# Optimization experiments

Hardware: AMD Instinct MI355X
Metric: run time of the kernel (lower is better)

## Reference

```python
import jax, jax.numpy as jnp
import numpy as np

B, QUE, VAL, D = 4, 128, 128, 512

def setup_inputs() -> dict:
    key = jax.random.key(0)
    k = jax.random.split(key, 8)
    return {
        "qs_1": jax.random.normal(k[0], (B, QUE, D), jnp.float32),
        "qs_2": jax.random.normal(k[1], (B, QUE, D), jnp.float32),  # unused by forward, kept for signature fidelity
        "ks":   jax.random.normal(k[2], (B, VAL, D), jnp.float32),
        "vs":   jax.random.normal(k[3], (B, VAL, D), jnp.float32),
        "sg_mask": jax.random.randint(k[4], (B, VAL), 0, 2).astype(bool),  # True = masked
        "W1":  jax.random.normal(k[5], (D, D), jnp.float32) / np.sqrt(D),
        "b1":  jnp.zeros((D,), jnp.float32),
        "Wse": jax.random.normal(k[6], (D, D), jnp.float32) / np.sqrt(D),
        "bse": jnp.zeros((D,), jnp.float32),
        "W2":  jax.random.normal(k[7], (D, 1), jnp.float32) / np.sqrt(D),
        "b2":  jnp.zeros((1,), jnp.float32),
    }

def reference(qs_1, qs_2, ks, vs, sg_mask, W1, b1, Wse, bse, W2, b2):
    # Pairwise query-key elementwise product: [B, que, val, d]
    x = qs_1[:, :, None, :] * ks[:, None, :, :]
    # linear1: Linear(d,d) + ReLU (dropout = identity at eval)
    h = jax.nn.relu(jnp.einsum('bqvd,de->bqve', x, W1) + b1)
    # linear2: Linear(d,1) + ReLU -> scalar score per (q, v) pair
    s = jax.nn.relu(jnp.einsum('bqvd,do->bqvo', h, W2) + b2)[..., 0]  # [B, que, val]
    m = sg_mask[:, None, :]                      # [B, 1, val], True = masked out
    # masked mean of h over the val axis (masked_fill(0) then divide by valid count)
    h = jnp.where(m[..., None], 0.0, h)
    denom = jnp.sum(~sg_mask, axis=-1).astype(h.dtype)      # [B]
    mean = h.sum(axis=2) / denom[:, None, None]             # [B, que, d]
    # squeeze-excitation gate: sigmoid(relu(Linear(d,d)))
    gate = jax.nn.sigmoid(jax.nn.relu(mean @ Wse + bse))    # [B, que, d]
    # masked softmax over val, weighted sum of values
    s = jnp.where(m, -1e9, s)
    w = jax.nn.softmax(s, axis=-1)                          # [B, que, val]
    out = jnp.einsum('bqv,bvd->bqd', w, vs)                 # [B, que, d]
    return gate * out
```

## Files before the change

kernel.cpp:

```cpp
#include <hip/hip_runtime.h>
#include <stdint.h>
#include <stddef.h>

#define BDIM 4
#define QUE  128
#define VAL  128
#define DD   512
#define BQ   (BDIM*QUE)
#define BK   64

typedef float    f32x4 __attribute__((ext_vector_type(4)));
typedef float    f32x2 __attribute__((ext_vector_type(2)));
typedef _Float16 f16x8 __attribute__((ext_vector_type(8)));
typedef _Float16 f16x4 __attribute__((ext_vector_type(4)));
typedef _Float16 f16x2 __attribute__((ext_vector_type(2)));

typedef const __attribute__((address_space(1))) void* gas_ptr;
typedef __attribute__((address_space(3))) void*       las_ptr;

__device__ __forceinline__ void async_copy16(const void* g, void* l) {
    __builtin_amdgcn_global_load_lds((gas_ptr)g, (las_ptr)l, 16, 0, 0);
}

__global__ __launch_bounds__(256) void prep_kernel(const float* __restrict__ W1,
                                                   _Float16* __restrict__ W1T,
                                                   const float* __restrict__ Wse,
                                                   _Float16* __restrict__ WseT,
                                                   const float* __restrict__ vs,
                                                   _Float16* __restrict__ vsT,
                                                   const float* __restrict__ qs1,
                                                   _Float16* __restrict__ qH,
                                                   const float* __restrict__ ks,
                                                   _Float16* __restrict__ ksH) {
    const int gx = blockIdx.x, gy = blockIdx.y;
    if (gy >= 36) {
        const float* src = (gy == 36) ? qs1 : ks;
        _Float16*    dst = (gy == 36) ? qH  : ksH;
        size_t base = (size_t)gx * 16384 + threadIdx.x * 4;
        #pragma unroll 4
        for (int i = 0; i < 16; ++i) {
            f32x4 w = *(const f32x4*)(src + base + (size_t)i * 1024);
            f16x4 h;
            h[0] = (_Float16)w[0]; h[1] = (_Float16)w[1];
            h[2] = (_Float16)w[2]; h[3] = (_Float16)w[3];
            *(f16x4*)(dst + base + (size_t)i * 1024) = h;
        }
        return;
    }
    __shared__ float tile[32][33];
    const int tx = threadIdx.x & 31;
    const int ty = threadIdx.x >> 5;
    if (gy < 32) {
        const float* src = (gy < 16) ? W1  : Wse;
        _Float16*    dst = (gy < 16) ? W1T : WseT;
        int a0 = gx * 32;
        int b0 = (gy & 15) * 32;
        #pragma unroll
        for (int r = 0; r < 4; ++r)
            tile[ty + r*8][tx] = src[(size_t)(a0 + ty + r*8) * DD + b0 + tx];
        __syncthreads();
        #pragma unroll
        for (int r = 0; r < 4; ++r) {
            int el = ty + r*8;
            dst[(size_t)(b0 + el) * DD + a0 + tx] = (_Float16)tile[tx][el];
        }
    } else {
        int bb = gy - 32;
        const float* src = vs  + (size_t)bb * VAL * DD;
        _Float16*    dst = vsT + (size_t)bb * DD * VAL;
        int b0 = gx * 32;
        for (int vt = 0; vt < 4; ++vt) {
            int a0 = vt * 32;
            __syncthreads();
            #pragma unroll
            for (int r = 0; r < 4; ++r)
                tile[ty + r*8][tx] = src[(size_t)(a0 + ty + r*8) * DD + b0 + tx];
            __syncthreads();
            #pragma unroll
            for (int r = 0; r < 4; ++r) {
                int el = ty + r*8;
                dst[(size_t)(b0 + el) * VAL + a0 + tx] = (_Float16)tile[tx][el];
            }
        }
    }
}

__global__ __launch_bounds__(256, 3) void gemm_h_kernel(
    const _Float16* __restrict__ qH,
    const _Float16* __restrict__ ksH,
    const int*   __restrict__ sgmask,
    const _Float16* __restrict__ W1T,
    const float* __restrict__ b1,
    const float* __restrict__ W2,
    float* __restrict__ s_part,
    float* __restrict__ meansum)
{
    __shared__ _Float16 Ah[2][128 * BK];
    __shared__ _Float16 Bh[128 * BK];
    __shared__ float sred[2][VAL];
    __shared__ float msumLDS[2][128];

    const int tid  = threadIdx.x;
    const int bq   = blockIdx.x;
    const int gy   = blockIdx.y;
    const int b    = bq >> 7;
    const int lane = tid & 63;
    const int wid  = tid >> 6;
    const int wm   = wid >> 1;
    const int wn   = wid & 1;
    const int quad = lane >> 4;
    const int lr   = lane & 15;

    f32x4 acc[4][4];
    #pragma unroll
    for (int i = 0; i < 4; ++i)
        #pragma unroll
        for (int j = 0; j < 4; ++j) acc[i][j] = (f32x4){0.f, 0.f, 0.f, 0.f};

    const int ar0 = tid >> 3;
    const int slt = tid & 7;
    const int ca0 = (slt - (ar0 & 7)) & 7;
    const _Float16* ksrow0 = ksH + ((size_t)b * VAL + ar0) * DD + ca0 * 8;
    const _Float16* qrow_g = qH  + (size_t)bq * DD + ca0 * 8;
    const int aoff0 = tid * 8;

    const int brow0 = tid >> 3;
    const int bc0   = ((tid & 7) - (brow0 & 7)) & 7;
    const _Float16* gB0 = W1T + (size_t)(gy * 128 + brow0) * DD + bc0 * 8;

    int faoff[4], fboff[4];
    #pragma unroll
    for (int mt = 0; mt < 4; ++mt) {
        int row = wm * 64 + mt * 16 + lr;
        faoff[mt] = row * BK + (((quad + row) & 7) << 3);
    }
    #pragma unroll
    for (int nt = 0; nt < 4; ++nt) {
        int row = wn * 64 + nt * 16 + lr;
        fboff[nt] = row * BK + (((quad + row) & 7) << 3);
    }

    #pragma unroll
    for (int j = 0; j < 4; ++j)
        async_copy16(gB0 + (size_t)j * 32 * DD, &Bh[(j * 256 + wid * 64) * 8]);
    f16x8 kv[4], qv;
    #pragma unroll
    for (int j = 0; j < 4; ++j)
        kv[j] = *(const f16x8*)(ksrow0 + (size_t)j * 32 * DD);
    qv = *(const f16x8*)(qrow_g);
    #pragma unroll
    for (int j = 0; j < 4; ++j)
        *(f16x8*)&Ah[0][aoff0 + j * 2048] = kv[j] * qv;
    #pragma unroll
    for (int j = 0; j < 4; ++j)
        kv[j] = *(const f16x8*)(ksrow0 + (size_t)j * 32 * DD + BK);
    qv = *(const f16x8*)(qrow_g + BK);
    __syncthreads();

    int p = 0;
    for (int i = 0; i < 8; ++i) {
        f16x8 fbr[2][4];
        #pragma unroll
        for (int s = 0; s < 2; ++s) {
            const int sx = s << 5;
            #pragma unroll
            for (int nt = 0; nt < 4; ++nt)
                fbr[s][nt] = *(const f16x8*)&Bh[fboff[nt] ^ sx];
        }
        asm volatile("s_waitcnt lgkmcnt(0)" ::: "memory");
        __builtin_amdgcn_s_barrier();

        if (i < 7) {
            const int kk = (i + 1) * BK;
            #pragma unroll
            for (int j = 0; j < 4; ++j)
                *(f16x8*)&Ah[p ^ 1][aoff0 + j * 2048] = kv[j] * qv;
            if (i < 6) {
                #pragma unroll
                for (int j = 0; j < 4; ++j)
                    kv[j] = *(const f16x8*)(ksrow0 + (size_t)j * 32 * DD + kk + BK);
                qv = *(const f16x8*)(qrow_g + kk + BK);
            }
            #pragma unroll
            for (int j = 0; j < 4; ++j)
                async_copy16(gB0 + (size_t)j * 32 * DD + kk,
                             &Bh[(j * 256 + wid * 64) * 8]);
        }

        const _Float16* Ab = &Ah[p][0];
        #pragma unroll
        for (int s = 0; s < 2; ++s) {
            const int sx = s << 5;
            f16x8 fa[4];
            #pragma unroll
            for (int mt = 0; mt < 4; ++mt)
                fa[mt] = *(const f16x8*)&Ab[faoff[mt] ^ sx];
            #pragma unroll
            for (int nt = 0; nt < 4; ++nt)
                #pragma unroll
                for (int mt = 0; mt < 4; ++mt)
                    acc[mt][nt] = __builtin_amdgcn_mfma_f32_16x16x32_f16(
                        fa[mt], fbr[s][nt], acc[mt][nt], 0, 0, 0);
        }
        __syncthreads();
        p ^= 1;
    }

    float b1v[4], w2v[4];
    #pragma unroll
    for (int nt = 0; nt < 4; ++nt) {
        int col = gy*128 + wn*64 + nt*16 + lr;
        b1v[nt] = b1[col];
        w2v[nt] = W2[col];
    }
    float msum[4] = {0.f, 0.f, 0.f, 0.f};
    #pragma unroll
    for (int mt = 0; mt < 4; ++mt) {
        #pragma unroll
        for (int reg = 0; reg < 4; ++reg) {
            int v = wm*64 + mt*16 + quad*4 + reg;
            int masked = sgmask[b * VAL + v];
            float sacc = 0.f;
            #pragma unroll
            for (int nt = 0; nt < 4; ++nt) {
                float h = acc[mt][nt][reg] + b1v[nt];
                h = fmaxf(h, 0.f);
                sacc += h * w2v[nt];
                if (!masked) msum[nt] += h;
            }
            sacc += __shfl_xor(sacc, 1);
            sacc += __shfl_xor(sacc, 2);
            sacc += __shfl_xor(sacc, 4);
            sacc += __shfl_xor(sacc, 8);
            if (lr == 0) sred[wn][v] = sacc;
        }
    }
    #pragma unroll
    for (int nt = 0; nt < 4; ++nt) {
        float m = msum[nt];
        m += __shfl_xor(m, 16);
        m += __shfl_xor(m, 32);
        if (lane < 16) msumLDS[wm][wn*64 + nt*16 + lr] = m;
    }
    __syncthreads();
    if (tid < 128) {
        s_part[((size_t)bq * 4 + gy) * VAL + tid] = sred[0][tid] + sred[1][tid];
    } else {
        int c = tid - 128;
        meansum[(size_t)bq * DD + gy*128 + c] = msumLDS[0][c] + msumLDS[1][c];
    }
}

#define MPAD 514
#define WPAD 130
__global__ __launch_bounds__(256) void final_kernel(
    const float* __restrict__ s_part,
    const float* __restrict__ msum,
    const int*   __restrict__ sgmask,
    const _Float16* __restrict__ WseT,
    const _Float16* __restrict__ vsT,
    const float* __restrict__ bse,
    const float* __restrict__ b2,
    float* __restrict__ out)
{
    __shared__ _Float16 meanLDS[32 * MPAD];
    __shared__ _Float16 wLDS[32 * WPAD];
    __shared__ _Float16 BLDS[32 * WPAD];

    const int tid  = threadIdx.x;
    const int q0   = blockIdx.x * 32;
    const int d0   = blockIdx.y * 32;
    const int b    = q0 >> 7;
    const int lane = tid & 63;
    const int wid  = tid >> 6;
    const int wm   = wid >> 1, wn = wid & 1;
    const int quad = lane >> 4;
    const int lr   = lane & 15;
    const int r    = tid >> 3;
    const int sl   = tid & 7;

    const float b2v = b2[0];
    const int   bq  = q0 + r;
    const float* sp = s_part + (size_t)bq * 4 * VAL;
    float vals[16];
    int   msk[16];
    float smax = -3.4e38f;
    #pragma unroll
    for (int i4 = 0; i4 < 4; ++i4) {
        f32x4 s0 = *(const f32x4*)(sp +           sl*16 + i4*4);
        f32x4 s1 = *(const f32x4*)(sp + VAL     + sl*16 + i4*4);
        f32x4 s2 = *(const f32x4*)(sp + 2*VAL   + sl*16 + i4*4);
        f32x4 s3 = *(const f32x4*)(sp + 3*VAL   + sl*16 + i4*4);
        #pragma unroll
        for (int j = 0; j < 4; ++j) {
            int idx = i4*4 + j;
            int v   = sl*16 + idx;
            float s = fmaxf(s0[j] + s1[j] + s2[j] + s3[j] + b2v, 0.f);
            int m   = sgmask[b * VAL + v];
            msk[idx] = m;
            if (m) s = -1e9f;
            vals[idx] = s;
            smax = fmaxf(smax, s);
        }
    }
    smax = fmaxf(smax, __shfl_xor(smax, 1));
    smax = fmaxf(smax, __shfl_xor(smax, 2));
    smax = fmaxf(smax, __shfl_xor(smax, 4));
    float sume = 0.f, cnt = 0.f;
    #pragma unroll
    for (int i = 0; i < 16; ++i) {
        vals[i] = __expf(vals[i] - smax);
        sume += vals[i];
        cnt  += msk[i] ? 0.f : 1.f;
    }
    sume += __shfl_xor(sume, 1);  cnt += __shfl_xor(cnt, 1);
    sume += __shfl_xor(sume, 2);  cnt += __shfl_xor(cnt, 2);
    sume += __shfl_xor(sume, 4);  cnt += __shfl_xor(cnt, 4);
    const float invse = 1.f / sume;
    const float invd  = 1.f / cnt;
    f16x8 wv0, wv1;
    #pragma unroll
    for (int i = 0; i < 8; ++i) {
        wv0[i] = (_Float16)(vals[i]     * invse);
        wv1[i] = (_Float16)(vals[i + 8] * invse);
    }
    *(f16x8*)&wLDS[r * WPAD + sl*16]     = wv0;
    *(f16x8*)&wLDS[r * WPAD + sl*16 + 8] = wv1;
    const float* mrow = msum + (size_t)bq * DD;
    #pragma unroll
    for (int i = 0; i < 8; ++i) {
        int e = i*64 + sl*8;
        f32x4 m0 = *(const f32x4*)(mrow + e);
        f32x4 m1 = *(const f32x4*)(mrow + e + 4);
        f16x8 mh;
        #pragma unroll
        for (int c = 0; c < 4; ++c) {
            mh[c]     = (_Float16)(m0[c] * invd);
            mh[c + 4] = (_Float16)(m1[c] * invd);
        }
        *(f16x8*)&meanLDS[r * MPAD + e] = mh;
    }
    __syncthreads();

    f32x4 accg = (f32x4){0.f, 0.f, 0.f, 0.f};
    const int a_off = (wm*16 + lr) * MPAD + quad*8;
    const int b_off = (wn*16 + lr) * WPAD + quad*8;
    const int st_off = r * WPAD + sl*16;
    #pragma unroll
    for (int cc = 0; cc < 4; ++cc) {
        const _Float16* wrow = WseT + (size_t)(d0 + r) * DD + cc*128 + sl*16;
        f16x8 bw0 = *(const f16x8*)(wrow);
        f16x8 bw1 = *(const f16x8*)(wrow + 8);
        *(f16x8*)&BLDS[st_off]     = bw0;
        *(f16x8*)&BLDS[st_off + 8] = bw1;
        __syncthreads();
        #pragma unroll
        for (int ks = 0; ks < 4; ++ks) {
            f16x8 fa = *(const f16x8*)&meanLDS[a_off + cc*128 + ks*32];
            f16x8 fb = *(const f16x8*)&BLDS[b_off + ks*32];
            accg = __builtin_amdgcn_mfma_f32_16x16x32_f16(fa, fb, accg, 0, 0, 0);
        }
        __syncthreads();
    }

    {
        const _Float16* vrow = vsT + ((size_t)b * DD + d0 + r) * VAL + sl*16;
        f16x8 bv0 = *(const f16x8*)(vrow);
        f16x8 bv1 = *(const f16x8*)(vrow + 8);
        *(f16x8*)&BLDS[st_off]     = bv0;
        *(f16x8*)&BLDS[st_off + 8] = bv1;
    }
    __syncthreads();
    f32x4 acco = (f32x4){0.f, 0.f, 0.f, 0.f};
    const int w_off = (wm*16 + lr) * WPAD + quad*8;
    #pragma unroll
    for (int ks = 0; ks < 4; ++ks) {
        f16x8 fa = *(const f16x8*)&wLDS[w_off + ks*32];
        f16x8 fb = *(const f16x8*)&BLDS[b_off + ks*32];
        acco = __builtin_amdgcn_mfma_f32_16x16x32_f16(fa, fb, acco, 0, 0, 0);
    }

    const int d = d0 + wn*16 + lr;
    const float bsev = bse[d];
    #pragma unroll
    for (int reg = 0; reg < 4; ++reg) {
        int q = q0 + wm*16 + quad*4 + reg;
        float g = fmaxf(accg[reg] + bsev, 0.f);
        g = 1.f / (1.f + __expf(-g));
        out[(size_t)q * DD + d] = g * acco[reg];
    }
}

extern "C" void kernel_launch(void* const* d_in, const int* in_sizes, int n_in,
                              void* d_out, int out_size, void* d_ws, size_t ws_size,
                              hipStream_t stream) {
    (void)in_sizes; (void)n_in; (void)out_size; (void)ws_size;
    const float* qs1 = (const float*)d_in[0];
    const float* ks  = (const float*)d_in[2];
    const float* vs  = (const float*)d_in[3];
    const int*   sg  = (const int*)d_in[4];
    const float* W1  = (const float*)d_in[5];
    const float* b1  = (const float*)d_in[6];
    const float* Wse = (const float*)d_in[7];
    const float* bse = (const float*)d_in[8];
    const float* W2  = (const float*)d_in[9];
    const float* b2  = (const float*)d_in[10];
    float* out = (float*)d_out;

    char* ws = (char*)d_ws;
    _Float16* W1T    = (_Float16*)(ws);
    _Float16* WseT   = (_Float16*)(ws + (512 << 10));
    _Float16* vsT    = (_Float16*)(ws + (1 << 20));
    float*    s_part = (float*)(ws + (1536 << 10));
    float*    msum   = (float*)(ws + (2560 << 10));
    _Float16* qH     = (_Float16*)(ws + (3584 << 10));
    _Float16* ksH    = (_Float16*)(ws + (4096 << 10));

    prep_kernel<<<dim3(16, 38), 256, 0, stream>>>(W1, W1T, Wse, WseT, vs, vsT,
                                                  qs1, qH, ks, ksH);
    gemm_h_kernel<<<dim3(BQ, 4), 256, 0, stream>>>(qH, ksH, sg, W1T, b1, W2, s_part, msum);
    final_kernel<<<dim3(16, 16), 256, 0, stream>>>(s_part, msum, sg, WseT, vsT, bse, b2, out);
}
```

Before: 130.4 us.

## Double-buffer W1 tile in LDS and use one barrier per k-step

Gives the B (W1T) tile two LDS buffers so the async global-to-LDS load of the next k-slice overlaps MFMA work on the current slice. This lets the main loop use a single vmcnt wait and barrier per iteration instead of the register-staged B fragments plus a trailing __syncthreads. The loop is fully unrolled with a peeled last iteration, and s_setprio raises wave priority around the MFMA bursts. In exchange LDS use grows and launch bounds drop from 3 to 2 blocks per CU, which reduces occupancy.

```diff
diff --git a/kernel.cpp b/kernel.cpp
--- a/kernel.cpp
+++ b/kernel.cpp
@@ -85,7 +85,7 @@
     }
 }
 
-__global__ __launch_bounds__(256, 3) void gemm_h_kernel(
+__global__ __launch_bounds__(256, 2) void gemm_h_kernel(
     const _Float16* __restrict__ qH,
     const _Float16* __restrict__ ksH,
     const int*   __restrict__ sgmask,
@@ -96,7 +96,7 @@
     float* __restrict__ meansum)
 {
     __shared__ _Float16 Ah[2][128 * BK];
-    __shared__ _Float16 Bh[128 * BK];
+    __shared__ _Float16 Bh[2][128 * BK];
     __shared__ float sred[2][VAL];
     __shared__ float msumLDS[2][128];
 
@@ -142,7 +142,8 @@
 
     #pragma unroll
     for (int j = 0; j < 4; ++j)
-        async_copy16(gB0 + (size_t)j * 32 * DD, &Bh[(j * 256 + wid * 64) * 8]);
+        async_copy16(gB0 + (size_t)j * 32 * DD, &Bh[0][(j * 256 + wid * 64) * 8]);
+    asm volatile("" ::: "memory");
     f16x8 kv[4], qv;
     #pragma unroll
     for (int j = 0; j < 4; ++j)
@@ -155,56 +156,83 @@
     for (int j = 0; j < 4; ++j)
         kv[j] = *(const f16x8*)(ksrow0 + (size_t)j * 32 * DD + BK);
     qv = *(const f16x8*)(qrow_g + BK);
-    __syncthreads();
+    asm volatile("" ::: "memory");
 
     int p = 0;
-    for (int i = 0; i < 8; ++i) {
-        f16x8 fbr[2][4];
+    #pragma unroll
+    for (int i = 0; i < 7; ++i) {
+        asm volatile("s_waitcnt vmcnt(5)" ::: "memory");
+        __builtin_amdgcn_s_barrier();
+
+        const int kk = (i + 1) * BK;
+        #pragma unroll
+        for (int j = 0; j < 4; ++j)
+            async_copy16(gB0 + (size_t)j * 32 * DD + kk,
+                         &Bh[p ^ 1][(j * 256 + wid * 64) * 8]);
+        asm volatile("" ::: "memory");
+
+        #pragma unroll
+        for (int j = 0; j < 4; ++j)
+            *(f16x8*)&Ah[p ^ 1][aoff0 + j * 2048] = kv[j] * qv;
+
+        if (i < 6) {
+            #pragma unroll
+            for (int j = 0; j < 4; ++j)
+                kv[j] = *(const f16x8*)(ksrow0 + (size_t)j * 32 * DD + kk + BK);
+            qv = *(const f16x8*)(qrow_g + kk + BK);
+        }
+        asm volatile("" ::: "memory");
+
+        const _Float16* Ab = &Ah[p][0];
+        const _Float16* Bb = &Bh[p][0];
         #pragma unroll
         for (int s = 0; s < 2; ++s) {
             const int sx = s << 5;
-            #pragma unroll
-            for (int nt = 0; nt < 4; ++nt)
-                fbr[s][nt] = *(const f16x8*)&Bh[fboff[nt] ^ sx];
-        }
-        asm volatile("s_waitcnt lgkmcnt(0)" ::: "memory");
-        __builtin_amdgcn_s_barrier();
-
-        if (i < 7) {
-            const int kk = (i + 1) * BK;
-            #pragma unroll
-            for (int j = 0; j < 4; ++j)
-                *(f16x8*)&Ah[p ^ 1][aoff0 + j * 2048] = kv[j] * qv;
-            if (i < 6) {
-                #pragma unroll
-                for (int j = 0; j < 4; ++j)
-                    kv[j] = *(const f16x8*)(ksrow0 + (size_t)j * 32 * DD + kk + BK);
-                qv = *(const f16x8*)(qrow_g + kk + BK);
-            }
-            #pragma unroll
-            for (int j = 0; j < 4; ++j)
-                async_copy16(gB0 + (size_t)j * 32 * DD + kk,
-                             &Bh[(j * 256 + wid * 64) * 8]);
-        }
-
-        const _Float16* Ab = &Ah[p][0];
-        #pragma unroll
-        for (int s = 0; s < 2; ++s) {
-            const int sx = s << 5;
-            f16x8 fa[4];
+            f16x8 fa[4], fb[4];
             #pragma unroll
             for (int mt = 0; mt < 4; ++mt)
                 fa[mt] = *(const f16x8*)&Ab[faoff[mt] ^ sx];
+            #pragma unroll
+            for (int nt = 0; nt < 4; ++nt)
+                fb[nt] = *(const f16x8*)&Bb[fboff[nt] ^ sx];
+            __builtin_amdgcn_s_setprio(1);
             #pragma unroll
             for (int nt = 0; nt < 4; ++nt)
                 #pragma unroll
                 for (int mt = 0; mt < 4; ++mt)
                     acc[mt][nt] = __builtin_amdgcn_mfma_f32_16x16x32_f16(
-                        fa[mt], fbr[s][nt], acc[mt][nt], 0, 0, 0);
-        }
-        __syncthreads();
+                        fa[mt], fb[nt], acc[mt][nt], 0, 0, 0);
+            __builtin_amdgcn_s_setprio(0);
+        }
         p ^= 1;
     }
+
+    asm volatile("s_waitcnt vmcnt(0)" ::: "memory");
+    __builtin_amdgcn_s_barrier();
+    {
+        const _Float16* Ab = &Ah[p][0];
+        const _Float16* Bb = &Bh[p][0];
+        #pragma unroll
+        for (int s = 0; s < 2; ++s) {
+            const int sx = s << 5;
+            f16x8 fa[4], fb[4];
+            #pragma unroll
+            for (int mt = 0; mt < 4; ++mt)
+                fa[mt] = *(const f16x8*)&Ab[faoff[mt] ^ sx];
+            #pragma unroll
+            for (int nt = 0; nt < 4; ++nt)
+                fb[nt] = *(const f16x8*)&Bb[fboff[nt] ^ sx];
+            __builtin_amdgcn_s_setprio(1);
+            #pragma unroll
+            for (int nt = 0; nt < 4; ++nt)
+                #pragma unroll
+                for (int mt = 0; mt < 4; ++mt)
+                    acc[mt][nt] = __builtin_amdgcn_mfma_f32_16x16x32_f16(
+                        fa[mt], fb[nt], acc[mt][nt], 0, 0, 0);
+            __builtin_amdgcn_s_setprio(0);
+        }
+    }
+    __syncthreads();
 
     float b1v[4], w2v[4];
     #pragma unroll
```

Result: slower. 138.5 us (+6.2%).
